# Performance work log

Measured on AMD Instinct MI355X. Metric: run time of the kernel, lower is better.

Reference implementation:

```python
import jax, jax.numpy as jnp
import numpy as np

BASE_THETA = 0.5
K_DOP = 0.2
K_NOR = 0.15
K_SERO = 0.1
DIM = 1024


def setup_inputs() -> dict:
    key = jax.random.key(0)
    ks = jax.random.split(key, 9)
    scale = 1.0 / np.sqrt(DIM)
    x = jax.random.normal(ks[0], (2, 2048, DIM), dtype=jnp.float32)
    Wq = jax.random.normal(ks[1], (DIM, DIM), dtype=jnp.float32) * scale
    bq = jnp.zeros((DIM,), dtype=jnp.float32)
    Wk = jax.random.normal(ks[2], (DIM, DIM), dtype=jnp.float32) * scale
    bk = jnp.zeros((DIM,), dtype=jnp.float32)
    Wv = jax.random.normal(ks[3], (DIM, DIM), dtype=jnp.float32) * scale
    bv = jnp.zeros((DIM,), dtype=jnp.float32)
    Wo = jax.random.normal(ks[4], (DIM, DIM), dtype=jnp.float32) * scale
    bo = jnp.zeros((DIM,), dtype=jnp.float32)
    return {"x": x, "Wq": Wq, "bq": bq, "Wk": Wk, "bk": bk,
            "Wv": Wv, "bv": bv, "Wo": Wo, "bo": bo}


def reference(x, Wq, bq, Wk, bk, Wv, bv, Wo, bo):
    # Projections: torch nn.Linear computes x @ W.T + b
    q = jnp.einsum('bsd,ed->bse', x, Wq) + bq
    k = jnp.einsum('bsd,ed->bse', x, Wk) + bk
    v = jnp.einsum('bsd,ed->bse', x, Wv) + bv
    # Full [B, S, S] scores (no 1/sqrt(d) scaling in the original)
    qk = jnp.einsum('bsd,btd->bst', q, k)
    theta = (BASE_THETA
             + K_DOP * jax.nn.sigmoid(qk)
             + K_NOR * jnp.tanh(qk)
             + K_SERO * jax.nn.relu(qk))
    attn = jax.nn.softmax(theta, axis=-1)
    out = jnp.einsum('bst,btd->bsd', attn, v)
    return jnp.einsum('bsd,ed->bse', out, Wo) + bo
```

## Files before the change

### kernel.cpp

```cpp
#include <hip/hip_runtime.h>
#include <hip/hip_fp16.h>
#include <stdint.h>

typedef _Float16 f16;
typedef __attribute__((ext_vector_type(8))) _Float16 f16x8;
typedef __attribute__((ext_vector_type(4))) _Float16 f16x4;
typedef __attribute__((ext_vector_type(4))) float f32x4;

#define SEQ 2048
#define DIM 1024
#define NBATCH 2
#define MTOT 4096

__global__ void fill_kernel(float* p, float v, int n){
  int i = blockIdx.x * 256 + threadIdx.x;
  if (i < n) p[i] = v;
}

__global__ void cvt_all(const float* __restrict__ x, const float* __restrict__ Wq,
                        const float* __restrict__ Wk, const float* __restrict__ Wv,
                        const float* __restrict__ Wo,
                        f16* __restrict__ x16, f16* __restrict__ Wcat, f16* __restrict__ Wo16,
                        float* __restrict__ rowacc){
  int b = blockIdx.x;
  if (b == 8192){
    float4 z = {0.f, 0.f, 0.f, 0.f};
#pragma unroll
    for (int i = 0; i < 4; i++) ((float4*)rowacc)[threadIdx.x + i * 256] = z;
    return;
  }
  const float* src; f16* dst; int i;
  if (b < 4096){
    src = x; dst = x16; i = b * 256 + threadIdx.x;
  } else {
    int t = (b - 4096) >> 10;
    i = ((b - 4096) & 1023) * 256 + threadIdx.x;
    src = t == 0 ? Wq : t == 1 ? Wk : t == 2 ? Wv : Wo;
    dst = (t == 3) ? Wo16 : Wcat + (size_t)t * DIM * DIM;
  }
  float4 v = ((const float4*)src)[i];
  ((f16x4*)dst)[i] = (f16x4){(f16)v.x, (f16)v.y, (f16)v.z, (f16)v.w};
}

#define GLOAD16(SRC, DST) __builtin_amdgcn_global_load_lds( \
    (__attribute__((address_space(1))) void*)(SRC), \
    (__attribute__((address_space(3))) void*)(DST), 16, 0, 0)

__device__ __forceinline__ float theta_exp(float v){
  const float e1 = __expf(-v);
  const float sg = 1.f / (1.f + e1);
  const float e2 = e1 * e1;
  const float th = 2.f / (1.f + e2) - 1.f;
  const float theta = 0.5f + 0.2f * sg + 0.15f * th + 0.1f * fmaxf(v, 0.f);
  return __expf(fminf(theta - 10.f, 11.f));
}

template<int MODE>
__global__ __launch_bounds__(256, 3)
void gemm256(const f16* __restrict__ A0, const f16* __restrict__ A1,
             const f16* __restrict__ B0,
             f16* __restrict__ O0, f16* __restrict__ O1,
             const float* __restrict__ c0, const float* __restrict__ c1,
             const float* __restrict__ c2, float* __restrict__ rowacc)
{
  __shared__ __align__(16) f16 As[8192];
  __shared__ __align__(16) f16 Bs[8192];
  const int tid  = threadIdx.x;
  const int lane = tid & 63;
  const int wid  = tid >> 6;

  int bm, bn, bz = 0, lda, ldb;
  const f16 *Ag, *Bg;
  bool isQK = true;
  if constexpr (MODE == 4){
    bm = blockIdx.x; bn = blockIdx.y; lda = DIM; ldb = DIM;
    Ag = A0; Bg = B0;
  } else {
    const int r = blockIdx.x;
    if (r < 512){
      bz = r >> 8; const int q = r & 255; bm = q & 15; bn = q >> 4;
      Ag = A0 + (long)bz * SEQ * 2048;
      Bg = A0 + DIM + (long)bz * SEQ * 2048;
      lda = 2048; ldb = 2048;
    } else {
      isQK = false;
      int q = r - 512; bz = q >> 7; q &= 127; bm = q & 15; bn = q >> 4;
      Ag = A1 + (long)bz * SEQ * DIM;
      Bg = B0;
      lda = DIM; ldb = DIM;
    }
  }

  const int s_r  = tid >> 3;
  const int s_cb = (tid & 7) ^ (s_r & 7);
  const f16* Ab = Ag + (long)(bm * 128 + s_r) * lda + s_cb * 8;
  const f16* Bb = Bg + (long)(bn * 128 + s_r) * ldb + s_cb * 8;

  const int l15 = lane & 15, l7 = lane & 7, lhi = lane >> 4;
  const int wrow = (wid >> 1) * 64;
  const int wcol = (wid & 1) * 64;
  const int ar = (wrow + l15) * 64;
  const int br = (wcol + l15) * 64;
  const int cb0 = ((0 + lhi) ^ l7) * 8;
  const int cb1 = ((4 + lhi) ^ l7) * 8;

  f32x4 acc[4][4] = {};

  for (int t = 0; t < 16; ++t){
    __syncthreads();
    GLOAD16(Ab + (long)t*64,                  &As[       tid*8]);
    GLOAD16(Ab + (long)t*64 + (long)32 * lda, &As[2048 + tid*8]);
    GLOAD16(Ab + (long)t*64 + (long)64 * lda, &As[4096 + tid*8]);
    GLOAD16(Ab + (long)t*64 + (long)96 * lda, &As[6144 + tid*8]);
    GLOAD16(Bb + (long)t*64,                  &Bs[       tid*8]);
    GLOAD16(Bb + (long)t*64 + (long)32 * ldb, &Bs[2048 + tid*8]);
    GLOAD16(Bb + (long)t*64 + (long)64 * ldb, &Bs[4096 + tid*8]);
    GLOAD16(Bb + (long)t*64 + (long)96 * ldb, &Bs[6144 + tid*8]);
    __syncthreads();
    f16x8 af[4], bf[4];
#pragma unroll
    for (int i = 0; i < 4; i++) af[i] = *(const f16x8*)&As[ar + i * 1024 + cb0];
#pragma unroll
    for (int j = 0; j < 4; j++) bf[j] = *(const f16x8*)&Bs[br + j * 1024 + cb0];
#pragma unroll
    for (int i = 0; i < 4; i++)
#pragma unroll
      for (int j = 0; j < 4; j++)
        acc[i][j] = __builtin_amdgcn_mfma_f32_16x16x32_f16(af[i], bf[j], acc[i][j], 0, 0, 0);
#pragma unroll
    for (int i = 0; i < 4; i++) af[i] = *(const f16x8*)&As[ar + i * 1024 + cb1];
#pragma unroll
    for (int j = 0; j < 4; j++) bf[j] = *(const f16x8*)&Bs[br + j * 1024 + cb1];
#pragma unroll
    for (int i = 0; i < 4; i++)
#pragma unroll
      for (int j = 0; j < 4; j++)
        acc[i][j] = __builtin_amdgcn_mfma_f32_16x16x32_f16(af[i], bf[j], acc[i][j], 0, 0, 0);
  }

  const int cc = l15;
  const int rr = lhi * 4;

  if constexpr (MODE == 4){
#pragma unroll
    for (int i = 0; i < 4; i++)
#pragma unroll
      for (int j = 0; j < 4; j++){
        const int col = bn * 128 + wcol + j * 16 + cc;
        if (col < 2048){
          const float badd = (col < 1024) ? c0[col] : c1[col - 1024];
#pragma unroll
          for (int r = 0; r < 4; r++){
            const int row = bm * 128 + wrow + i * 16 + rr + r;
            O0[(long)row * 2048 + col] = (f16)(acc[i][j][r] + badd);
          }
        } else {
          const int dcol = col - 2048;
          const float badd = c2[dcol];
#pragma unroll
          for (int r = 0; r < 4; r++){
            const int row = bm * 128 + wrow + i * 16 + rr + r;
            O1[(long)row * DIM + dcol] = (f16)(acc[i][j][r] + badd);
          }
        }
      }
  } else {
    if (isQK){
#pragma unroll
      for (int i = 0; i < 4; i++)
#pragma unroll
        for (int r = 0; r < 4; r++){
          const int row = bm * 128 + wrow + i * 16 + rr + r;
          float rs = 0.f;
#pragma unroll
          for (int j = 0; j < 4; j++){
            const int col = bn * 128 + wcol + j * 16 + cc;
            const float P = theta_exp(acc[i][j][r]);
            O0[(long)bz * SEQ * SEQ + (long)row * SEQ + col] = (f16)P;
            rs += P;
          }
          rs += __shfl_xor(rs, 1, 64);
          rs += __shfl_xor(rs, 2, 64);
          rs += __shfl_xor(rs, 4, 64);
          rs += __shfl_xor(rs, 8, 64);
          if (cc == 0) atomicAdd(&rowacc[bz * SEQ + row], rs);
        }
    } else {
#pragma unroll
      for (int i = 0; i < 4; i++)
#pragma unroll
        for (int j = 0; j < 4; j++){
          const int col = bn * 128 + wcol + j * 16 + cc;
          const int row0 = bm * 128 + wrow + i * 16 + rr;
          f16x4 pk = {(f16)acc[i][j][0], (f16)acc[i][j][1],
                      (f16)acc[i][j][2], (f16)acc[i][j][3]};
          *(f16x4*)&O1[(long)bz * DIM * SEQ + (long)col * SEQ + row0] = pk;
        }
    }
  }
}

__global__ __launch_bounds__(512, 2)
void gemm512_final(const f16* __restrict__ Pb, const f16* __restrict__ Vw,
                   float* __restrict__ out, const float* __restrict__ bo,
                   const float* __restrict__ rowacc)
{
  __shared__ __align__(16) f16 As[8192];
  __shared__ __align__(16) f16 Bs[8192];
  const int tid  = threadIdx.x;
  const int lane = tid & 63;
  const int wid  = tid >> 6;
  const int bm = blockIdx.x, bn = blockIdx.y, bz = blockIdx.z;

  const f16* Ag = Pb + (long)bz * SEQ * SEQ;
  const f16* Bg = Vw + (long)bz * DIM * SEQ;

  const int s_r  = tid >> 3;
  const int s_cb = (tid & 7) ^ (s_r & 7);
  const f16* Ab = Ag + (long)(bm * 128 + s_r) * SEQ + s_cb * 8;
  const f16* Bb = Bg + (long)(bn * 128 + s_r) * SEQ + s_cb * 8;

  const int l15 = lane & 15, l7 = lane & 7, lhi = lane >> 4;
  const int wrow = (wid >> 2) * 64;
  const int wcol = (wid & 3) * 32;
  const int ar = (wrow + l15) * 64;
  const int br = (wcol + l15) * 64;
  const int cb0 = ((0 + lhi) ^ l7) * 8;
  const int cb1 = ((4 + lhi) ^ l7) * 8;

  f32x4 acc[4][2] = {};

  for (int t = 0; t < 32; ++t){
    __syncthreads();
    GLOAD16(Ab + (long)t*64,                  &As[       tid*8]);
    GLOAD16(Ab + (long)t*64 + (long)64 * SEQ, &As[4096 + tid*8]);
    GLOAD16(Bb + (long)t*64,                  &Bs[       tid*8]);
    GLOAD16(Bb + (long)t*64 + (long)64 * SEQ, &Bs[4096 + tid*8]);
    __syncthreads();
    f16x8 af[4], bf[2];
#pragma unroll
    for (int i = 0; i < 4; i++) af[i] = *(const f16x8*)&As[ar + i * 1024 + cb0];
#pragma unroll
    for (int j = 0; j < 2; j++) bf[j] = *(const f16x8*)&Bs[br + j * 1024 + cb0];
#pragma unroll
    for (int i = 0; i < 4; i++)
#pragma unroll
      for (int j = 0; j < 2; j++)
        acc[i][j] = __builtin_amdgcn_mfma_f32_16x16x32_f16(af[i], bf[j], acc[i][j], 0, 0, 0);
#pragma unroll
    for (int i = 0; i < 4; i++) af[i] = *(const f16x8*)&As[ar + i * 1024 + cb1];
#pragma unroll
    for (int j = 0; j < 2; j++) bf[j] = *(const f16x8*)&Bs[br + j * 1024 + cb1];
#pragma unroll
    for (int i = 0; i < 4; i++)
#pragma unroll
      for (int j = 0; j < 2; j++)
        acc[i][j] = __builtin_amdgcn_mfma_f32_16x16x32_f16(af[i], bf[j], acc[i][j], 0, 0, 0);
  }

  const int cc = l15;
  const int rr = lhi * 4;
#pragma unroll
  for (int i = 0; i < 4; i++)
#pragma unroll
    for (int r = 0; r < 4; r++){
      const int row = bm * 128 + wrow + i * 16 + rr + r;
      const float inv = 1.f / rowacc[bz * SEQ + row];
#pragma unroll
      for (int j = 0; j < 2; j++){
        const int col = bn * 128 + wcol + j * 16 + cc;
        out[(long)bz * SEQ * DIM + (long)row * DIM + col] = acc[i][j][r] * inv + bo[col];
      }
    }
}

extern "C" void kernel_launch(void* const* d_in, const int* in_sizes, int n_in,
                              void* d_out, int out_size, void* d_ws, size_t ws_size,
                              hipStream_t stream){
  const float* x  = (const float*)d_in[0];
  const float* Wq = (const float*)d_in[1];
  const float* bq = (const float*)d_in[2];
  const float* Wk = (const float*)d_in[3];
  const float* bk = (const float*)d_in[4];
  const float* Wv = (const float*)d_in[5];
  const float* bv = (const float*)d_in[6];
  const float* Wo = (const float*)d_in[7];
  const float* bo = (const float*)d_in[8];
  float* out = (float*)d_out;

  char* ws = (char*)d_ws;
  size_t off = 0;
  auto alloc = [&](size_t bytes) -> char* {
    char* p = ws + off; off += (bytes + 255) & ~(size_t)255; return p;
  };

  f16* x16     = (f16*)alloc(2ull * MTOT * DIM);
  f16* Wcat    = (f16*)alloc(2ull * 3 * DIM * DIM);
  f16* Wo16    = (f16*)alloc(2ull * DIM * DIM);
  f16* qkcat   = (f16*)alloc(2ull * MTOT * 2 * DIM);
  f16* vbuf    = (f16*)alloc(2ull * MTOT * DIM);
  f16* Pbuf    = (f16*)alloc(2ull * NBATCH * SEQ * SEQ);
  f16* vWoT    = (f16*)alloc(2ull * NBATCH * DIM * SEQ);
  float* rowac = (float*)alloc(4ull * MTOT);

  if (off > ws_size){
    fill_kernel<<<(out_size + 255) / 256, 256, 0, stream>>>(out, 12345.0f, out_size);
    return;
  }

  cvt_all<<<8193, 256, 0, stream>>>(x, Wq, Wk, Wv, Wo, x16, Wcat, Wo16, rowac);

  gemm256<4><<<dim3(MTOT / 128, 3 * DIM / 128, 1), 256, 0, stream>>>(
      x16, nullptr, Wcat, qkcat, vbuf, bq, bk, bv, nullptr);

  gemm256<7><<<768, 256, 0, stream>>>(
      qkcat, vbuf, Wo16, Pbuf, vWoT, nullptr, nullptr, nullptr, rowac);

  gemm512_final<<<dim3(SEQ / 128, DIM / 128, NBATCH), 512, 0, stream>>>(
      Pbuf, vWoT, out, bo, rowac);
}
```

Measured before the change: 119.5 us.

## Split final PV GEMM over K halves and retile QK blocks for more parallelism

The final P·(VWo) GEMM is split along the sequence (K) dimension into two halves, each written as fp32 partial sums. A new combine kernel adds the halves, applies the row normalisation and adds the bias. The QK score blocks shrink from 128x128 to 128x64 tiles, so the merged kernel launches more blocks, and launch bounds are raised to allow higher occupancy. This trades an extra 32 MB of fp32 partial traffic plus one more launch for better SM fill in the final GEMM, which previously had only 256 blocks.

```diff
diff --git a/kernel.cpp b/kernel.cpp
--- a/kernel.cpp
+++ b/kernel.cpp
@@ -55,46 +55,23 @@
   return __expf(fminf(theta - 10.f, 11.f));
 }
 
-template<int MODE>
 __global__ __launch_bounds__(256, 3)
-void gemm256(const f16* __restrict__ A0, const f16* __restrict__ A1,
-             const f16* __restrict__ B0,
-             f16* __restrict__ O0, f16* __restrict__ O1,
-             const float* __restrict__ c0, const float* __restrict__ c1,
-             const float* __restrict__ c2, float* __restrict__ rowacc)
+void gemm_qkv(const f16* __restrict__ A0, const f16* __restrict__ B0,
+              f16* __restrict__ O0, f16* __restrict__ O1,
+              const float* __restrict__ c0, const float* __restrict__ c1,
+              const float* __restrict__ c2)
 {
   __shared__ __align__(16) f16 As[8192];
   __shared__ __align__(16) f16 Bs[8192];
   const int tid  = threadIdx.x;
   const int lane = tid & 63;
   const int wid  = tid >> 6;
-
-  int bm, bn, bz = 0, lda, ldb;
-  const f16 *Ag, *Bg;
-  bool isQK = true;
-  if constexpr (MODE == 4){
-    bm = blockIdx.x; bn = blockIdx.y; lda = DIM; ldb = DIM;
-    Ag = A0; Bg = B0;
-  } else {
-    const int r = blockIdx.x;
-    if (r < 512){
-      bz = r >> 8; const int q = r & 255; bm = q & 15; bn = q >> 4;
-      Ag = A0 + (long)bz * SEQ * 2048;
-      Bg = A0 + DIM + (long)bz * SEQ * 2048;
-      lda = 2048; ldb = 2048;
-    } else {
-      isQK = false;
-      int q = r - 512; bz = q >> 7; q &= 127; bm = q & 15; bn = q >> 4;
-      Ag = A1 + (long)bz * SEQ * DIM;
-      Bg = B0;
-      lda = DIM; ldb = DIM;
-    }
-  }
+  const int bm = blockIdx.x, bn = blockIdx.y;
 
   const int s_r  = tid >> 3;
   const int s_cb = (tid & 7) ^ (s_r & 7);
-  const f16* Ab = Ag + (long)(bm * 128 + s_r) * lda + s_cb * 8;
-  const f16* Bb = Bg + (long)(bn * 128 + s_r) * ldb + s_cb * 8;
+  const f16* Ab = A0 + (long)(bm * 128 + s_r) * DIM + s_cb * 8;
+  const f16* Bb = B0 + (long)(bn * 128 + s_r) * DIM + s_cb * 8;
 
   const int l15 = lane & 15, l7 = lane & 7, lhi = lane >> 4;
   const int wrow = (wid >> 1) * 64;
@@ -109,13 +86,13 @@
   for (int t = 0; t < 16; ++t){
     __syncthreads();
     GLOAD16(Ab + (long)t*64,                  &As[       tid*8]);
-    GLOAD16(Ab + (long)t*64 + (long)32 * lda, &As[2048 + tid*8]);
-    GLOAD16(Ab + (long)t*64 + (long)64 * lda, &As[4096 + tid*8]);
-    GLOAD16(Ab + (long)t*64 + (long)96 * lda, &As[6144 + tid*8]);
+    GLOAD16(Ab + (long)t*64 + (long)32 * DIM, &As[2048 + tid*8]);
+    GLOAD16(Ab + (long)t*64 + (long)64 * DIM, &As[4096 + tid*8]);
+    GLOAD16(Ab + (long)t*64 + (long)96 * DIM, &As[6144 + tid*8]);
     GLOAD16(Bb + (long)t*64,                  &Bs[       tid*8]);
-    GLOAD16(Bb + (long)t*64 + (long)32 * ldb, &Bs[2048 + tid*8]);
-    GLOAD16(Bb + (long)t*64 + (long)64 * ldb, &Bs[4096 + tid*8]);
-    GLOAD16(Bb + (long)t*64 + (long)96 * ldb, &Bs[6144 + tid*8]);
+    GLOAD16(Bb + (long)t*64 + (long)32 * DIM, &Bs[2048 + tid*8]);
+    GLOAD16(Bb + (long)t*64 + (long)64 * DIM, &Bs[4096 + tid*8]);
+    GLOAD16(Bb + (long)t*64 + (long)96 * DIM, &Bs[6144 + tid*8]);
     __syncthreads();
     f16x8 af[4], bf[4];
 #pragma unroll
@@ -140,138 +117,266 @@
 
   const int cc = l15;
   const int rr = lhi * 4;
-
-  if constexpr (MODE == 4){
-#pragma unroll
-    for (int i = 0; i < 4; i++)
-#pragma unroll
-      for (int j = 0; j < 4; j++){
-        const int col = bn * 128 + wcol + j * 16 + cc;
-        if (col < 2048){
-          const float badd = (col < 1024) ? c0[col] : c1[col - 1024];
-#pragma unroll
-          for (int r = 0; r < 4; r++){
-            const int row = bm * 128 + wrow + i * 16 + rr + r;
-            O0[(long)row * 2048 + col] = (f16)(acc[i][j][r] + badd);
-          }
-        } else {
-          const int dcol = col - 2048;
-          const float badd = c2[dcol];
-#pragma unroll
-          for (int r = 0; r < 4; r++){
-            const int row = bm * 128 + wrow + i * 16 + rr + r;
-            O1[(long)row * DIM + dcol] = (f16)(acc[i][j][r] + badd);
-          }
+#pragma unroll
+  for (int i = 0; i < 4; i++)
+#pragma unroll
+    for (int j = 0; j < 4; j++){
+      const int col = bn * 128 + wcol + j * 16 + cc;
+      if (col < 2048){
+        const float badd = (col < 1024) ? c0[col] : c1[col - 1024];
+#pragma unroll
+        for (int r = 0; r < 4; r++){
+          const int row = bm * 128 + wrow + i * 16 + rr + r;
+          O0[(long)row * 2048 + col] = (f16)(acc[i][j][r] + badd);
+        }
+      } else {
+        const int dcol = col - 2048;
+        const float badd = c2[dcol];
+#pragma unroll
+        for (int r = 0; r < 4; r++){
+          const int row = bm * 128 + wrow + i * 16 + rr + r;
+          O1[(long)row * DIM + dcol] = (f16)(acc[i][j][r] + badd);
         }
       }
-  } else {
-    if (isQK){
-#pragma unroll
-      for (int i = 0; i < 4; i++)
-#pragma unroll
-        for (int r = 0; r < 4; r++){
-          const int row = bm * 128 + wrow + i * 16 + rr + r;
-          float rs = 0.f;
-#pragma unroll
-          for (int j = 0; j < 4; j++){
-            const int col = bn * 128 + wcol + j * 16 + cc;
-            const float P = theta_exp(acc[i][j][r]);
-            O0[(long)bz * SEQ * SEQ + (long)row * SEQ + col] = (f16)P;
-            rs += P;
-          }
-          rs += __shfl_xor(rs, 1, 64);
-          rs += __shfl_xor(rs, 2, 64);
-          rs += __shfl_xor(rs, 4, 64);
-          rs += __shfl_xor(rs, 8, 64);
-          if (cc == 0) atomicAdd(&rowacc[bz * SEQ + row], rs);
-        }
-    } else {
-#pragma unroll
-      for (int i = 0; i < 4; i++)
-#pragma unroll
-        for (int j = 0; j < 4; j++){
-          const int col = bn * 128 + wcol + j * 16 + cc;
-          const int row0 = bm * 128 + wrow + i * 16 + rr;
-          f16x4 pk = {(f16)acc[i][j][0], (f16)acc[i][j][1],
-                      (f16)acc[i][j][2], (f16)acc[i][j][3]};
-          *(f16x4*)&O1[(long)bz * DIM * SEQ + (long)col * SEQ + row0] = pk;
-        }
     }
-  }
-}
-
-__global__ __launch_bounds__(512, 2)
-void gemm512_final(const f16* __restrict__ Pb, const f16* __restrict__ Vw,
-                   float* __restrict__ out, const float* __restrict__ bo,
-                   const float* __restrict__ rowacc)
+}
+
+__global__ __launch_bounds__(256, 5)
+void gemm_merged(const f16* __restrict__ qkcat, const f16* __restrict__ vbuf,
+                 const f16* __restrict__ Wo16,
+                 f16* __restrict__ Pbuf, f16* __restrict__ vWoT,
+                 float* __restrict__ rowacc)
 {
   __shared__ __align__(16) f16 As[8192];
   __shared__ __align__(16) f16 Bs[8192];
   const int tid  = threadIdx.x;
   const int lane = tid & 63;
   const int wid  = tid >> 6;
-  const int bm = blockIdx.x, bn = blockIdx.y, bz = blockIdx.z;
-
-  const f16* Ag = Pb + (long)bz * SEQ * SEQ;
-  const f16* Bg = Vw + (long)bz * DIM * SEQ;
-
+  const int l15 = lane & 15, l7 = lane & 7, lhi = lane >> 4;
   const int s_r  = tid >> 3;
   const int s_cb = (tid & 7) ^ (s_r & 7);
-  const f16* Ab = Ag + (long)(bm * 128 + s_r) * SEQ + s_cb * 8;
-  const f16* Bb = Bg + (long)(bn * 128 + s_r) * SEQ + s_cb * 8;
+  const int cb0 = ((0 + lhi) ^ l7) * 8;
+  const int cb1 = ((4 + lhi) ^ l7) * 8;
+  const int cc = l15, rr = lhi * 4;
+  const int r = blockIdx.x;
+
+  if (r < 1024){
+    const int bz = r >> 9, q = r & 511, bm = q >> 5, bn = q & 31;
+    const f16* Ag = qkcat + (long)bz * SEQ * 2048;
+    const f16* Bg = qkcat + DIM + (long)bz * SEQ * 2048;
+    const f16* Ab = Ag + (long)(bm * 128 + s_r) * 2048 + s_cb * 8;
+    const f16* Bb = Bg + (long)(bn * 64  + s_r) * 2048 + s_cb * 8;
+
+    const int wrow = (wid >> 1) * 64;
+    const int wcol = (wid & 1) * 32;
+    const int ar = (wrow + l15) * 64;
+    const int br = (wcol + l15) * 64;
+
+    f32x4 acc[4][2] = {};
+
+    for (int t = 0; t < 16; ++t){
+      __syncthreads();
+      GLOAD16(Ab + (long)t*64,                   &As[       tid*8]);
+      GLOAD16(Ab + (long)t*64 + (long)32 * 2048, &As[2048 + tid*8]);
+      GLOAD16(Ab + (long)t*64 + (long)64 * 2048, &As[4096 + tid*8]);
+      GLOAD16(Ab + (long)t*64 + (long)96 * 2048, &As[6144 + tid*8]);
+      GLOAD16(Bb + (long)t*64,                   &Bs[       tid*8]);
+      GLOAD16(Bb + (long)t*64 + (long)32 * 2048, &Bs[2048 + tid*8]);
+      __syncthreads();
+      f16x8 af[4], bf[2];
+#pragma unroll
+      for (int i = 0; i < 4; i++) af[i] = *(const f16x8*)&As[ar + i * 1024 + cb0];
+#pragma unroll
+      for (int j = 0; j < 2; j++) bf[j] = *(const f16x8*)&Bs[br + j * 1024 + cb0];
+#pragma unroll
+      for (int i = 0; i < 4; i++)
+#pragma unroll
+        for (int j = 0; j < 2; j++)
+          acc[i][j] = __builtin_amdgcn_mfma_f32_16x16x32_f16(af[i], bf[j], acc[i][j], 0, 0, 0);
+#pragma unroll
+      for (int i = 0; i < 4; i++) af[i] = *(const f16x8*)&As[ar + i * 1024 + cb1];
+#pragma unroll
+      for (int j = 0; j < 2; j++) bf[j] = *(const f16x8*)&Bs[br + j * 1024 + cb1];
+#pragma unroll
+      for (int i = 0; i < 4; i++)
+#pragma unroll
+        for (int j = 0; j < 2; j++)
+          acc[i][j] = __builtin_amdgcn_mfma_f32_16x16x32_f16(af[i], bf[j], acc[i][j], 0, 0, 0);
+    }
+
+#pragma unroll
+    for (int i = 0; i < 4; i++)
+#pragma unroll
+      for (int rq = 0; rq < 4; rq++){
+        const int row = bm * 128 + wrow + i * 16 + rr + rq;
+        float rs = 0.f;
+#pragma unroll
+        for (int j = 0; j < 2; j++){
+          const int col = bn * 64 + wcol + j * 16 + cc;
+          const float P = theta_exp(acc[i][j][rq]);
+          Pbuf[(long)bz * SEQ * SEQ + (long)row * SEQ + col] = (f16)P;
+          rs += P;
+        }
+        rs += __shfl_xor(rs, 1, 64);
+        rs += __shfl_xor(rs, 2, 64);
+        rs += __shfl_xor(rs, 4, 64);
+        rs += __shfl_xor(rs, 8, 64);
+        if (cc == 0) atomicAdd(&rowacc[bz * SEQ + row], rs);
+      }
+  } else {
+    const int q = r - 1024;
+    const int bz = q >> 7, qq = q & 127, bm = qq & 15, bn = qq >> 4;
+    const f16* Ag = vbuf + (long)bz * SEQ * DIM;
+    const f16* Ab = Ag + (long)(bm * 128 + s_r) * DIM + s_cb * 8;
+    const f16* Bb = Wo16 + (long)(bn * 128 + s_r) * DIM + s_cb * 8;
+
+    const int wrow = (wid >> 1) * 64;
+    const int wcol = (wid & 1) * 64;
+    const int ar = (wrow + l15) * 64;
+    const int br = (wcol + l15) * 64;
+
+    f32x4 acc[4][4] = {};
+
+    for (int t = 0; t < 16; ++t){
+      __syncthreads();
+      GLOAD16(Ab + (long)t*64,                  &As[       tid*8]);
+      GLOAD16(Ab + (long)t*64 + (long)32 * DIM, &As[2048 + tid*8]);
+      GLOAD16(Ab + (long)t*64 + (long)64 * DIM, &As[4096 + tid*8]);
+      GLOAD16(Ab + (long)t*64 + (long)96 * DIM, &As[6144 + tid*8]);
+      GLOAD16(Bb + (long)t*64,                  &Bs[       tid*8]);
+      GLOAD16(Bb + (long)t*64 + (long)32 * DIM, &Bs[2048 + tid*8]);
+      GLOAD16(Bb + (long)t*64 + (long)64 * DIM, &Bs[4096 + tid*8]);
+      GLOAD16(Bb + (long)t*64 + (long)96 * DIM, &Bs[6144 + tid*8]);
+      __syncthreads();
+      f16x8 af[4], bf[4];
+#pragma unroll
+      for (int i = 0; i < 4; i++) af[i] = *(const f16x8*)&As[ar + i * 1024 + cb0];
+#pragma unroll
+      for (int j = 0; j < 4; j++) bf[j] = *(const f16x8*)&Bs[br + j * 1024 + cb0];
+#pragma unroll
+      for (int i = 0; i < 4; i++)
+#pragma unroll
+        for (int j = 0; j < 4; j++)
+          acc[i][j] = __builtin_amdgcn_mfma_f32_16x16x32_f16(af[i], bf[j], acc[i][j], 0, 0, 0);
+#pragma unroll
+      for (int i = 0; i < 4; i++) af[i] = *(const f16x8*)&As[ar + i * 1024 + cb1];
+#pragma unroll
+      for (int j = 0; j < 4; j++) bf[j] = *(const f16x8*)&Bs[br + j * 1024 + cb1];
+#pragma unroll
+      for (int i = 0; i < 4; i++)
+#pragma unroll
+        for (int j = 0; j < 4; j++)
+          acc[i][j] = __builtin_amdgcn_mfma_f32_16x16x32_f16(af[i], bf[j], acc[i][j], 0, 0, 0);
+    }
+
+#pragma unroll
+    for (int i = 0; i < 4; i++)
+#pragma unroll
+      for (int j = 0; j < 4; j++){
+        const int col = bn * 128 + wcol + j * 16 + cc;
+        const int row0 = bm * 128 + wrow + i * 16 + rr;
+        f16x4 pk = {(f16)acc[i][j][0], (f16)acc[i][j][1],
+                    (f16)acc[i][j][2], (f16)acc[i][j][3]};
+        *(f16x4*)&vWoT[(long)bz * DIM * SEQ + (long)col * SEQ + row0] = pk;
+      }
+  }
+}
+
+__global__ __launch_bounds__(256, 4)
+void gemm_final(const f16* __restrict__ Pb, const f16* __restrict__ Vw,
+                float* __restrict__ psum)
+{
+  __shared__ __align__(16) f16 As[8192];
+  __shared__ __align__(16) f16 Bs[8192];
+  const int tid  = threadIdx.x;
+  const int lane = tid & 63;
+  const int wid  = tid >> 6;
+  const int bm = blockIdx.x, bn = blockIdx.y;
+  const int bz = blockIdx.z >> 1, kh = blockIdx.z & 1;
+
+  const f16* Ag = Pb + (long)bz * SEQ * SEQ + (long)kh * 1024;
+  const f16* Bg = Vw + (long)bz * DIM * SEQ + (long)kh * 1024;
+
+  const int s_r  = tid >> 3;
+  const int s_cb = (tid & 7) ^ (s_r & 7);
+  const f16* Ab = Ag + (long)(bm * 128 + s_r) * 2048 + s_cb * 8;
+  const f16* Bb = Bg + (long)(bn * 128 + s_r) * 2048 + s_cb * 8;
 
   const int l15 = lane & 15, l7 = lane & 7, lhi = lane >> 4;
-  const int wrow = (wid >> 2) * 64;
-  const int wcol = (wid & 3) * 32;
+  const int wrow = (wid >> 1) * 64;
+  const int wcol = (wid & 1) * 64;
   const int ar = (wrow + l15) * 64;
   const int br = (wcol + l15) * 64;
   const int cb0 = ((0 + lhi) ^ l7) * 8;
   const int cb1 = ((4 + lhi) ^ l7) * 8;
 
-  f32x4 acc[4][2] = {};
-
-  for (int t = 0; t < 32; ++t){
+  f32x4 acc[4][4] = {};
+
+  for (int t = 0; t < 16; ++t){
     __syncthreads();
-    GLOAD16(Ab + (long)t*64,                  &As[       tid*8]);
-    GLOAD16(Ab + (long)t*64 + (long)64 * SEQ, &As[4096 + tid*8]);
-    GLOAD16(Bb + (long)t*64,                  &Bs[       tid*8]);
-    GLOAD16(Bb + (long)t*64 + (long)64 * SEQ, &Bs[4096 + tid*8]);
+    GLOAD16(Ab + (long)t*64,                   &As[       tid*8]);
+    GLOAD16(Ab + (long)t*64 + (long)32 * 2048, &As[2048 + tid*8]);
+    GLOAD16(Ab + (long)t*64 + (long)64 * 2048, &As[4096 + tid*8]);
+    GLOAD16(Ab + (long)t*64 + (long)96 * 2048, &As[6144 + tid*8]);
+    GLOAD16(Bb + (long)t*64,                   &Bs[       tid*8]);
+    GLOAD16(Bb + (long)t*64 + (long)32 * 2048, &Bs[2048 + tid*8]);
+    GLOAD16(Bb + (long)t*64 + (long)64 * 2048, &Bs[4096 + tid*8]);
+    GLOAD16(Bb + (long)t*64 + (long)96 * 2048, &Bs[6144 + tid*8]);
     __syncthreads();
-    f16x8 af[4], bf[2];
+    f16x8 af[4], bf[4];
 #pragma unroll
     for (int i = 0; i < 4; i++) af[i] = *(const f16x8*)&As[ar + i * 1024 + cb0];
 #pragma unroll
-    for (int j = 0; j < 2; j++) bf[j] = *(const f16x8*)&Bs[br + j * 1024 + cb0];
-#pragma unroll
-    for (int i = 0; i < 4; i++)
-#pragma unroll
-      for (int j = 0; j < 2; j++)
+    for (int j = 0; j < 4; j++) bf[j] = *(const f16x8*)&Bs[br + j * 1024 + cb0];
+#pragma unroll
+    for (int i = 0; i < 4; i++)
+#pragma unroll
+      for (int j = 0; j < 4; j++)
         acc[i][j] = __builtin_amdgcn_mfma_f32_16x16x32_f16(af[i], bf[j], acc[i][j], 0, 0, 0);
 #pragma unroll
     for (int i = 0; i < 4; i++) af[i] = *(const f16x8*)&As[ar + i * 1024 + cb1];
 #pragma unroll
-    for (int j = 0; j < 2; j++) bf[j] = *(const f16x8*)&Bs[br + j * 1024 + cb1];
-#pragma unroll
-    for (int i = 0; i < 4; i++)
-#pragma unroll
-      for (int j = 0; j < 2; j++)
+    for (int j = 0; j < 4; j++) bf[j] = *(const f16x8*)&Bs[br + j * 1024 + cb1];
+#pragma unroll
+    for (int i = 0; i < 4; i++)
+#pragma unroll
+      for (int j = 0; j < 4; j++)
         acc[i][j] = __builtin_amdgcn_mfma_f32_16x16x32_f16(af[i], bf[j], acc[i][j], 0, 0, 0);
   }
 
   const int cc = l15;
   const int rr = lhi * 4;
+  float* Po = psum + (long)kh * MTOT * DIM + (long)bz * SEQ * DIM;
 #pragma unroll
   for (int i = 0; i < 4; i++)
 #pragma unroll
-    for (int r = 0; r < 4; r++){
-      const int row = bm * 128 + wrow + i * 16 + rr + r;
-      const float inv = 1.f / rowacc[bz * SEQ + row];
-#pragma unroll
-      for (int j = 0; j < 2; j++){
-        const int col = bn * 128 + wcol + j * 16 + cc;
-        out[(long)bz * SEQ * DIM + (long)row * DIM + col] = acc[i][j][r] * inv + bo[col];
+    for (int j = 0; j < 4; j++){
+      const int col = bn * 128 + wcol + j * 16 + cc;
+#pragma unroll
+      for (int r = 0; r < 4; r++){
+        const int row = bm * 128 + wrow + i * 16 + rr + r;
+        Po[(long)row * DIM + col] = acc[i][j][r];
       }
     }
+}
+
+__global__ __launch_bounds__(256)
+void combine_kernel(const float* __restrict__ psum, const float* __restrict__ rowacc,
+                    const float* __restrict__ bo, float* __restrict__ out)
+{
+  const long i = (long)blockIdx.x * 256 + threadIdx.x;
+  const int row = (int)(i >> 8);
+  const int c4  = (int)(i & 255);
+  float4 a = ((const float4*)psum)[i];
+  float4 b = ((const float4*)(psum + (size_t)MTOT * DIM))[i];
+  float4 bb = ((const float4*)bo)[c4];
+  const float inv = 1.f / rowacc[row];
+  float4 o;
+  o.x = (a.x + b.x) * inv + bb.x;
+  o.y = (a.y + b.y) * inv + bb.y;
+  o.z = (a.z + b.z) * inv + bb.z;
+  o.w = (a.w + b.w) * inv + bb.w;
+  ((float4*)out)[i] = o;
 }
 
 extern "C" void kernel_launch(void* const* d_in, const int* in_sizes, int n_in,
@@ -302,6 +407,7 @@
   f16* Pbuf    = (f16*)alloc(2ull * NBATCH * SEQ * SEQ);
   f16* vWoT    = (f16*)alloc(2ull * NBATCH * DIM * SEQ);
   float* rowac = (float*)alloc(4ull * MTOT);
+  float* psum  = (float*)alloc(4ull * 2 * MTOT * DIM);
 
   if (off > ws_size){
     fill_kernel<<<(out_size + 255) / 256, 256, 0, stream>>>(out, 12345.0f, out_size);
@@ -310,12 +416,13 @@
 
   cvt_all<<<8193, 256, 0, stream>>>(x, Wq, Wk, Wv, Wo, x16, Wcat, Wo16, rowac);
 
-  gemm256<4><<<dim3(MTOT / 128, 3 * DIM / 128, 1), 256, 0, stream>>>(
-      x16, nullptr, Wcat, qkcat, vbuf, bq, bk, bv, nullptr);
-
-  gemm256<7><<<768, 256, 0, stream>>>(
-      qkcat, vbuf, Wo16, Pbuf, vWoT, nullptr, nullptr, nullptr, rowac);
-
-  gemm512_final<<<dim3(SEQ / 128, DIM / 128, NBATCH), 512, 0, stream>>>(
-      Pbuf, vWoT, out, bo, rowac);
-}
+  gemm_qkv<<<dim3(MTOT / 128, 3 * DIM / 128, 1), 256, 0, stream>>>(
+      x16, Wcat, qkcat, vbuf, bq, bk, bv);
+
+  gemm_merged<<<1280, 256, 0, stream>>>(qkcat, vbuf, Wo16, Pbuf, vWoT, rowac);
+
+  gemm_final<<<dim3(SEQ / 128, DIM / 128, 2 * NBATCH), 256, 0, stream>>>(
+      Pbuf, vWoT, psum);
+
+  combine_kernel<<<MTOT * DIM / 4 / 256, 256, 0, stream>>>(psum, rowac, bo, out);
+}
```

Result: slower. 128.9 us (+7.9%).
